# Performance work log

Hardware: AMD Instinct MI355X
Metric: run time of the kernel (lower is better)

The kernel has to match this reference:

```python
import jax, jax.numpy as jnp
from jax import lax
import numpy as np

IN, HID, OUT = 28, 64, 10


def _lstm_layer(x_seq, W_ih, W_hh, b_ih, b_hh):
    # x_seq: [B, T, in]; PyTorch gate order: i, f, g, o (stacked along 4H)
    B = x_seq.shape[0]
    H = W_hh.shape[1]
    # Precompute input projection for all timesteps: [B, T, 4H]
    x_proj = jnp.einsum('bti,gi->btg', x_seq, W_ih) + b_ih + b_hh

    def step(carry, xt):
        h, c = carry
        gates = xt + h @ W_hh.T  # [B, 4H]
        i, f, g, o = jnp.split(gates, 4, axis=-1)
        i = jax.nn.sigmoid(i)
        f = jax.nn.sigmoid(f)
        g = jnp.tanh(g)
        o = jax.nn.sigmoid(o)
        c = f * c + i * g
        h = o * jnp.tanh(c)
        return (h, c), h

    h0 = jnp.zeros((B, H), x_seq.dtype)
    (_, _), hs = lax.scan(step, (h0, h0), jnp.swapaxes(x_proj, 0, 1))
    return jnp.swapaxes(hs, 0, 1)  # [B, T, H]


def setup_inputs() -> dict:
    key = jax.random.key(0)
    ks = jax.random.split(key, 12)
    s_in = 1.0 / np.sqrt(HID)
    u = lambda k, shape: jax.random.uniform(k, shape, jnp.float32, -s_in, s_in)
    return {
        'x': jax.random.normal(ks[0], (16384, 1, 28, 28), jnp.float32),
        'W_ih0': u(ks[1], (4 * HID, IN)),
        'W_hh0': u(ks[2], (4 * HID, HID)),
        'b_ih0': u(ks[3], (4 * HID,)),
        'b_hh0': u(ks[4], (4 * HID,)),
        'W_ih1': u(ks[5], (4 * HID, HID)),
        'W_hh1': u(ks[6], (4 * HID, HID)),
        'b_ih1': u(ks[7], (4 * HID,)),
        'b_hh1': u(ks[8], (4 * HID,)),
        'W_lin': u(ks[9], (OUT, HID)),
        'b_lin': u(ks[10], (OUT,)),
    }


def reference(x, W_ih0, W_hh0, b_ih0, b_hh0, W_ih1, W_hh1, b_ih1, b_hh1, W_lin, b_lin):
    # (N, C, H, W) -> (N, C*H, W): sequence of rows, feature = W = 28
    x = x.reshape(x.shape[0], -1, x.shape[-1])
    h1 = _lstm_layer(x, W_ih0, W_hh0, b_ih0, b_hh0)   # [B, T, 64]
    h2 = _lstm_layer(h1, W_ih1, W_hh1, b_ih1, b_hh1)  # [B, T, 64]
    last = h2[:, -1, :]
    return last @ W_lin.T + b_lin  # [B, 10]
```

## Files before the change

### kernel.cpp

```cpp
#include <hip/hip_runtime.h>


typedef _Float16 half8 __attribute__((ext_vector_type(8)));
typedef float floatx4 __attribute__((ext_vector_type(4)));

#define NFRAG 112
#define WS_BIAS_OFF (NFRAG * 1024)
#define K2 2.8853900817779268f

#if __has_builtin(__builtin_amdgcn_exp2f)
#define EXP2(v) __builtin_amdgcn_exp2f(v)
#else
#define EXP2(v) __expf(0.6931471805599453f * (v))
#endif
#define RCP(v) __builtin_amdgcn_rcpf(v)

__global__ void prep_kernel(const float* __restrict__ Wih0, const float* __restrict__ Whh0,
                            const float* __restrict__ bih0, const float* __restrict__ bhh0,
                            const float* __restrict__ Wih1, const float* __restrict__ Whh1,
                            const float* __restrict__ bih1, const float* __restrict__ bhh1,
                            _Float16* __restrict__ wA, float* __restrict__ wBias) {
    int idx = blockIdx.x * blockDim.x + threadIdx.x;
    if (idx < NFRAG * 512) {
        int f = idx >> 9, slot = idx & 511;
        int lane = slot >> 3, j = slot & 7;
        int mt, kt, layer;
        if (f < 48) { layer = 0; mt = f / 3; kt = f % 3; }
        else        { layer = 1; int f2 = f - 48; mt = f2 >> 2; kt = f2 & 3; }
        int m = mt * 16 + (lane & 15);
        int k = kt * 32 + (lane >> 4) * 8 + j;
        int u = m >> 2, g = m & 3;
        int row = g * 64 + u;
        float v;
        if (layer == 0) {
            if (k < 28)       v = Wih0[row * 28 + k];
            else if (k == 28) v = bih0[row] + bhh0[row];
            else if (k < 32)  v = 0.f;
            else              v = Whh0[row * 64 + (k - 32)];
        } else {
            if (k < 64)       v = Wih1[row * 64 + k];
            else              v = Whh1[row * 64 + (k - 64)];
        }
        float s = (g == 2) ? K2 : -1.4426950408889634f;
        wA[idx] = (_Float16)(v * s);
    } else if (idx < NFRAG * 512 + 256) {
        int m = idx - NFRAG * 512;
        int g = m & 3;
        int row = g * 64 + (m >> 2);
        float s = (g == 2) ? K2 : -1.4426950408889634f;
        wBias[m] = (bih1[row] + bhh1[row]) * s;
    }
}

__device__ __forceinline__ void gate4(const floatx4* acc, float* c,
                                      _Float16* plane, const int* offs) {
    float ei[4], ef[4], eg[4], eo[4];
    #pragma unroll
    for (int i = 0; i < 4; ++i) {
        floatx4 a = acc[i];
        ei[i] = EXP2(a[0]);
        ef[i] = EXP2(a[1]);
        eg[i] = EXP2(a[2]);
        eo[i] = EXP2(a[3]);
    }
    float num[4], rd[4], po[4];
    #pragma unroll
    for (int i = 0; i < 4; ++i) {
        float pi = 1.0f + ei[i];
        float pf = 1.0f + ef[i];
        float pg = 1.0f + eg[i];
        po[i] = 1.0f + eo[i];
        float m = pg * pi;
        num[i] = c[i] * m + (eg[i] - 1.0f) * pf;
        rd[i]  = RCP(pf * m);
    }
    float ec[4];
    #pragma unroll
    for (int i = 0; i < 4; ++i) {
        float cn = num[i] * rd[i];
        c[i] = cn;
        ec[i] = EXP2(K2 * cn);
    }
    #pragma unroll
    for (int i = 0; i < 4; ++i) {
        float r2 = RCP(ec[i] * po[i] + po[i]);
        plane[offs[i]] = (_Float16)((ec[i] - 1.0f) * r2);
    }
}

__launch_bounds__(256, 2)
__global__ void lstm_mfma(const float* __restrict__ x,
                          const _Float16* __restrict__ wA,
                          const float* __restrict__ wBias,
                          const float* __restrict__ Wlin, const float* __restrict__ blin,
                          float* __restrict__ out) {
    __shared__ __align__(16) _Float16 h0p[2][2048];
    __shared__ __align__(16) _Float16 h1p[2][2048];
    __shared__ __align__(16) _Float16 xb[2][1024];
    __shared__ float wlin_s[640];
    __shared__ float blin_s[10];

    const int lane = threadIdx.x;
    const int w    = threadIdx.y;
    const int tid  = w * 64 + lane;
    const int quad = lane >> 4;
    const int col  = lane & 15;
    const int l8   = lane * 8;

    half8 A0[4][3], A1[4][4];
    floatx4 bias1[4];
    int hwr0[4];
    #pragma unroll
    for (int j = 0; j < 4; ++j) {
        const int MT = 4 * w + j;
        #pragma unroll
        for (int kt = 0; kt < 3; ++kt)
            A0[j][kt] = *(const half8*)(wA + (MT * 3 + kt) * 512 + l8);
        #pragma unroll
        for (int kt = 0; kt < 4; ++kt)
            A1[j][kt] = *(const half8*)(wA + (48 + MT * 4 + kt) * 512 + l8);
        const int u = MT * 4 + quad;
        bias1[j] = *(const floatx4*)(wBias + u * 4);
        hwr0[j] = (u >> 5) * 512 + (((u >> 3) & 3) * 16 + col) * 8 + (u & 7);
    }

    const int ks = tid & 31;
    const int cs = tid >> 5;
    const bool xvalid = ks < 28;
    const bool xone   = (ks == 28);
    const float* xg = x + (blockIdx.x * 32 + cs) * 784 + ks;
    const int xstg0 = ((ks >> 3) * 16 + cs) * 8 + (ks & 7);

    {
        #pragma unroll
        for (int k = 0; k < 4; ++k) {
            ((int*)&h0p[1][0])[tid * 4 + k] = 0;
            ((int*)&h1p[1][0])[tid * 4 + k] = 0;
        }
        #pragma unroll
        for (int s = 0; s < 4; ++s) {
            float xv = xvalid ? xg[s * 8 * 784] : 0.f;
            xb[0][xstg0 + (s & 1) * 64 + (s >> 1) * 512] =
                xone ? (_Float16)1.0f : (_Float16)xv;
        }
    }
    __syncthreads();

    float c0[2][4] = {{0.f, 0.f, 0.f, 0.f}, {0.f, 0.f, 0.f, 0.f}};
    float c1[2][4] = {{0.f, 0.f, 0.f, 0.f}, {0.f, 0.f, 0.f, 0.f}};

    for (int p = -1; p <= 27; ++p) {
        const int pr  = p & 1;
        const int pr1 = pr ^ 1;
        const bool doL0 = (p < 27);
        const bool doL1 = (p >= 0);

        float xn[4] = {0.f, 0.f, 0.f, 0.f};
        if (p <= 25 && xvalid) {
            const float* xgp = xg + (p + 2) * 28;
            #pragma unroll
            for (int s = 0; s < 4; ++s) xn[s] = xgp[s * 8 * 784];
        }

        #pragma unroll
        for (int in = 0; in < 2; ++in) {
            const int hb = in * 1024;

            half8 bh0[2];
            #pragma unroll
            for (int kt = 0; kt < 2; ++kt)
                bh0[kt] = *(const half8*)&h0p[pr][hb + kt * 512 + l8];

            int offs[4];
            #pragma unroll
            for (int j = 0; j < 4; ++j) offs[j] = hwr0[j] + hb;

            if (doL0) {
                half8 bx = *(const half8*)&xb[pr1][in * 512 + l8];
                floatx4 acc0[4];
                #pragma unroll
                for (int j = 0; j < 4; ++j) {
                    acc0[j] = __builtin_amdgcn_mfma_f32_16x16x32_f16(
                                  A0[j][0], bx, (floatx4){0.f, 0.f, 0.f, 0.f}, 0, 0, 0);
                    #pragma unroll
                    for (int kt = 0; kt < 2; ++kt)
                        acc0[j] = __builtin_amdgcn_mfma_f32_16x16x32_f16(
                                      A0[j][kt + 1], bh0[kt], acc0[j], 0, 0, 0);
                }
                if (doL1) {
                    floatx4 acc1[4];
                    half8 bh1[2];
                    #pragma unroll
                    for (int kt = 0; kt < 2; ++kt)
                        bh1[kt] = *(const half8*)&h1p[pr1][hb + kt * 512 + l8];
                    #pragma unroll
                    for (int j = 0; j < 4; ++j) {
                        acc1[j] = bias1[j];
                        #pragma unroll
                        for (int kt = 0; kt < 2; ++kt)
                            acc1[j] = __builtin_amdgcn_mfma_f32_16x16x32_f16(
                                          A1[j][kt], bh0[kt], acc1[j], 0, 0, 0);
                        #pragma unroll
                        for (int kt = 0; kt < 2; ++kt)
                            acc1[j] = __builtin_amdgcn_mfma_f32_16x16x32_f16(
                                          A1[j][kt + 2], bh1[kt], acc1[j], 0, 0, 0);
                    }
                    gate4(acc0, c0[in], &h0p[pr1][0], offs);
                    gate4(acc1, c1[in], &h1p[pr][0], offs);
                } else {
                    gate4(acc0, c0[in], &h0p[pr1][0], offs);
                }
            } else {
                floatx4 acc1[4];
                half8 bh1[2];
                #pragma unroll
                for (int kt = 0; kt < 2; ++kt)
                    bh1[kt] = *(const half8*)&h1p[pr1][hb + kt * 512 + l8];
                #pragma unroll
                for (int j = 0; j < 4; ++j) {
                    acc1[j] = bias1[j];
                    #pragma unroll
                    for (int kt = 0; kt < 2; ++kt)
                        acc1[j] = __builtin_amdgcn_mfma_f32_16x16x32_f16(
                                      A1[j][kt], bh0[kt], acc1[j], 0, 0, 0);
                    #pragma unroll
                    for (int kt = 0; kt < 2; ++kt)
                        acc1[j] = __builtin_amdgcn_mfma_f32_16x16x32_f16(
                                      A1[j][kt + 2], bh1[kt], acc1[j], 0, 0, 0);
                }
                gate4(acc1, c1[in], &h1p[pr][0], offs);
            }
        }

        if (p <= 25) {
            #pragma unroll
            for (int s = 0; s < 4; ++s)
                xb[pr][xstg0 + (s & 1) * 64 + (s >> 1) * 512] =
                    xone ? (_Float16)1.0f : (_Float16)xn[s];
        }
        __syncthreads();
    }

    wlin_s[tid]       = Wlin[tid];
    wlin_s[tid + 256] = Wlin[tid + 256];
    if (tid < 128) wlin_s[tid + 512] = Wlin[tid + 512];
    if (tid < 10)  blin_s[tid] = blin[tid];
    __syncthreads();
    for (int e = tid; e < 320; e += 256) {
        int b = e / 10, o = e - b * 10;
        float a = blin_s[o];
        #pragma unroll 8
        for (int uu = 0; uu < 64; ++uu) {
            float hv = (float)h1p[1][((b >> 4) * 2 + (uu >> 5)) * 512 + (((uu >> 3) & 3) * 16 + (b & 15)) * 8 + (uu & 7)];
            a += wlin_s[o * 64 + uu] * hv;
        }
        out[(blockIdx.x * 32 + b) * 10 + o] = a;
    }
}

extern "C" void kernel_launch(void* const* d_in, const int* in_sizes, int n_in,
                              void* d_out, int out_size, void* d_ws, size_t ws_size,
                              hipStream_t stream) {
    const float* x    = (const float*)d_in[0];
    const float* Wih0 = (const float*)d_in[1];
    const float* Whh0 = (const float*)d_in[2];
    const float* bih0 = (const float*)d_in[3];
    const float* bhh0 = (const float*)d_in[4];
    const float* Wih1 = (const float*)d_in[5];
    const float* Whh1 = (const float*)d_in[6];
    const float* bih1 = (const float*)d_in[7];
    const float* bhh1 = (const float*)d_in[8];
    const float* Wlin = (const float*)d_in[9];
    const float* blin = (const float*)d_in[10];
    float* out = (float*)d_out;

    _Float16* wA    = (_Float16*)d_ws;
    float*    wBias = (float*)((char*)d_ws + WS_BIAS_OFF);

    prep_kernel<<<225, 256, 0, stream>>>(Wih0, Whh0, bih0, bhh0,
                                         Wih1, Whh1, bih1, bhh1, wA, wBias);
    lstm_mfma<<<512, dim3(64, 4), 0, stream>>>(x, wA, wBias, Wlin, blin, out);
}
```

Baseline: 177.2 us.

## Split gate rows over 8 waves per block with 16 sequences each

Each block now handles 16 sequences with 8 waves instead of 32 sequences with 4 waves, so each wave owns 2 gate tiles rather than 4. Per-wave weight registers and the serial per-step work shrink, which lets more blocks sit on a CU (launch bounds 512,8) and shortens the recurrent critical path. Layer-0 and layer-1 gate activations are batched into one gate call to interleave the transcendental work. In exchange, each block does fewer MFMAs per barrier, barriers now span twice as many waves, and the register cap from 8 blocks per CU may force spills.

```diff
diff --git a/kernel.cpp b/kernel.cpp
--- a/kernel.cpp
+++ b/kernel.cpp
@@ -52,20 +52,21 @@
     }
 }
 
-__device__ __forceinline__ void gate4(const floatx4* acc, float* c,
-                                      _Float16* plane, const int* offs) {
-    float ei[4], ef[4], eg[4], eo[4];
-    #pragma unroll
-    for (int i = 0; i < 4; ++i) {
+template <int N>
+__device__ __forceinline__ void gate_batch(const floatx4* acc, float* c,
+                                           _Float16* const* planes, const int* offs) {
+    float ei[N], ef[N], eg[N], eo[N];
+    #pragma unroll
+    for (int i = 0; i < N; ++i) {
         floatx4 a = acc[i];
         ei[i] = EXP2(a[0]);
         ef[i] = EXP2(a[1]);
         eg[i] = EXP2(a[2]);
         eo[i] = EXP2(a[3]);
     }
-    float num[4], rd[4], po[4];
-    #pragma unroll
-    for (int i = 0; i < 4; ++i) {
+    float num[N], rd[N], po[N];
+    #pragma unroll
+    for (int i = 0; i < N; ++i) {
         float pi = 1.0f + ei[i];
         float pf = 1.0f + ef[i];
         float pg = 1.0f + eg[i];
@@ -74,29 +75,29 @@
         num[i] = c[i] * m + (eg[i] - 1.0f) * pf;
         rd[i]  = RCP(pf * m);
     }
-    float ec[4];
-    #pragma unroll
-    for (int i = 0; i < 4; ++i) {
+    float ec[N];
+    #pragma unroll
+    for (int i = 0; i < N; ++i) {
         float cn = num[i] * rd[i];
         c[i] = cn;
         ec[i] = EXP2(K2 * cn);
     }
     #pragma unroll
-    for (int i = 0; i < 4; ++i) {
+    for (int i = 0; i < N; ++i) {
         float r2 = RCP(ec[i] * po[i] + po[i]);
-        plane[offs[i]] = (_Float16)((ec[i] - 1.0f) * r2);
-    }
-}
-
-__launch_bounds__(256, 2)
+        planes[i][offs[i]] = (_Float16)((ec[i] - 1.0f) * r2);
+    }
+}
+
+__launch_bounds__(512, 8)
 __global__ void lstm_mfma(const float* __restrict__ x,
                           const _Float16* __restrict__ wA,
                           const float* __restrict__ wBias,
                           const float* __restrict__ Wlin, const float* __restrict__ blin,
                           float* __restrict__ out) {
-    __shared__ __align__(16) _Float16 h0p[2][2048];
-    __shared__ __align__(16) _Float16 h1p[2][2048];
-    __shared__ __align__(16) _Float16 xb[2][1024];
+    __shared__ __align__(16) _Float16 h0p[2][1024];
+    __shared__ __align__(16) _Float16 h1p[2][1024];
+    __shared__ __align__(16) _Float16 xb[2][512];
     __shared__ float wlin_s[640];
     __shared__ float blin_s[10];
 
@@ -107,12 +108,12 @@
     const int col  = lane & 15;
     const int l8   = lane * 8;
 
-    half8 A0[4][3], A1[4][4];
-    floatx4 bias1[4];
-    int hwr0[4];
-    #pragma unroll
-    for (int j = 0; j < 4; ++j) {
-        const int MT = 4 * w + j;
+    half8 A0[2][3], A1[2][4];
+    floatx4 bias1[2];
+    int hwr[2];
+    #pragma unroll
+    for (int j = 0; j < 2; ++j) {
+        const int MT = 2 * w + j;
         #pragma unroll
         for (int kt = 0; kt < 3; ++kt)
             A0[j][kt] = *(const half8*)(wA + (MT * 3 + kt) * 512 + l8);
@@ -121,33 +122,26 @@
             A1[j][kt] = *(const half8*)(wA + (48 + MT * 4 + kt) * 512 + l8);
         const int u = MT * 4 + quad;
         bias1[j] = *(const floatx4*)(wBias + u * 4);
-        hwr0[j] = (u >> 5) * 512 + (((u >> 3) & 3) * 16 + col) * 8 + (u & 7);
+        hwr[j] = (u >> 5) * 512 + (((u >> 3) & 3) * 16 + col) * 8 + (u & 7);
     }
 
     const int ks = tid & 31;
     const int cs = tid >> 5;
     const bool xvalid = ks < 28;
     const bool xone   = (ks == 28);
-    const float* xg = x + (blockIdx.x * 32 + cs) * 784 + ks;
-    const int xstg0 = ((ks >> 3) * 16 + cs) * 8 + (ks & 7);
+    const float* xg = x + (blockIdx.x * 16 + cs) * 784 + ks;
+    const int xstg = ((ks >> 3) * 16 + cs) * 8 + (ks & 7);
 
     {
-        #pragma unroll
-        for (int k = 0; k < 4; ++k) {
-            ((int*)&h0p[1][0])[tid * 4 + k] = 0;
-            ((int*)&h1p[1][0])[tid * 4 + k] = 0;
-        }
-        #pragma unroll
-        for (int s = 0; s < 4; ++s) {
-            float xv = xvalid ? xg[s * 8 * 784] : 0.f;
-            xb[0][xstg0 + (s & 1) * 64 + (s >> 1) * 512] =
-                xone ? (_Float16)1.0f : (_Float16)xv;
-        }
+        ((int*)&h0p[1][0])[tid] = 0;
+        ((int*)&h1p[1][0])[tid] = 0;
+        float xv = xvalid ? xg[0] : 0.f;
+        xb[0][xstg] = xone ? (_Float16)1.0f : (_Float16)xv;
     }
     __syncthreads();
 
-    float c0[2][4] = {{0.f, 0.f, 0.f, 0.f}, {0.f, 0.f, 0.f, 0.f}};
-    float c1[2][4] = {{0.f, 0.f, 0.f, 0.f}, {0.f, 0.f, 0.f, 0.f}};
+    float c0[2] = {0.f, 0.f};
+    float c1[2] = {0.f, 0.f};
 
     for (int p = -1; p <= 27; ++p) {
         const int pr  = p & 1;
@@ -155,106 +149,85 @@
         const bool doL0 = (p < 27);
         const bool doL1 = (p >= 0);
 
-        float xn[4] = {0.f, 0.f, 0.f, 0.f};
-        if (p <= 25 && xvalid) {
-            const float* xgp = xg + (p + 2) * 28;
-            #pragma unroll
-            for (int s = 0; s < 4; ++s) xn[s] = xgp[s * 8 * 784];
-        }
-
+        float xn = 0.f;
+        if (p <= 25 && xvalid) xn = xg[(p + 2) * 28];
+
+        half8 bx, bh0[2];
+        if (doL0) bx = *(const half8*)&xb[pr1][l8];
         #pragma unroll
-        for (int in = 0; in < 2; ++in) {
-            const int hb = in * 1024;
-
-            half8 bh0[2];
-            #pragma unroll
-            for (int kt = 0; kt < 2; ++kt)
-                bh0[kt] = *(const half8*)&h0p[pr][hb + kt * 512 + l8];
-
-            int offs[4];
-            #pragma unroll
-            for (int j = 0; j < 4; ++j) offs[j] = hwr0[j] + hb;
-
-            if (doL0) {
-                half8 bx = *(const half8*)&xb[pr1][in * 512 + l8];
-                floatx4 acc0[4];
-                #pragma unroll
-                for (int j = 0; j < 4; ++j) {
-                    acc0[j] = __builtin_amdgcn_mfma_f32_16x16x32_f16(
-                                  A0[j][0], bx, (floatx4){0.f, 0.f, 0.f, 0.f}, 0, 0, 0);
-                    #pragma unroll
-                    for (int kt = 0; kt < 2; ++kt)
-                        acc0[j] = __builtin_amdgcn_mfma_f32_16x16x32_f16(
-                                      A0[j][kt + 1], bh0[kt], acc0[j], 0, 0, 0);
-                }
-                if (doL1) {
-                    floatx4 acc1[4];
-                    half8 bh1[2];
-                    #pragma unroll
-                    for (int kt = 0; kt < 2; ++kt)
-                        bh1[kt] = *(const half8*)&h1p[pr1][hb + kt * 512 + l8];
-                    #pragma unroll
-                    for (int j = 0; j < 4; ++j) {
-                        acc1[j] = bias1[j];
-                        #pragma unroll
-                        for (int kt = 0; kt < 2; ++kt)
-                            acc1[j] = __builtin_amdgcn_mfma_f32_16x16x32_f16(
-                                          A1[j][kt], bh0[kt], acc1[j], 0, 0, 0);
-                        #pragma unroll
-                        for (int kt = 0; kt < 2; ++kt)
-                            acc1[j] = __builtin_amdgcn_mfma_f32_16x16x32_f16(
-                                          A1[j][kt + 2], bh1[kt], acc1[j], 0, 0, 0);
-                    }
-                    gate4(acc0, c0[in], &h0p[pr1][0], offs);
-                    gate4(acc1, c1[in], &h1p[pr][0], offs);
-                } else {
-                    gate4(acc0, c0[in], &h0p[pr1][0], offs);
-                }
-            } else {
-                floatx4 acc1[4];
-                half8 bh1[2];
+        for (int kt = 0; kt < 2; ++kt)
+            bh0[kt] = *(const half8*)&h0p[pr][kt * 512 + l8];
+
+        floatx4 acc0[2], acc1[2];
+        if (doL0) {
+            #pragma unroll
+            for (int j = 0; j < 2; ++j) {
+                acc0[j] = __builtin_amdgcn_mfma_f32_16x16x32_f16(
+                              A0[j][0], bx, (floatx4){0.f, 0.f, 0.f, 0.f}, 0, 0, 0);
                 #pragma unroll
                 for (int kt = 0; kt < 2; ++kt)
-                    bh1[kt] = *(const half8*)&h1p[pr1][hb + kt * 512 + l8];
+                    acc0[j] = __builtin_amdgcn_mfma_f32_16x16x32_f16(
+                                  A0[j][kt + 1], bh0[kt], acc0[j], 0, 0, 0);
+            }
+        }
+        if (doL1) {
+            #pragma unroll
+            for (int j = 0; j < 2; ++j) {
+                acc1[j] = bias1[j];
                 #pragma unroll
-                for (int j = 0; j < 4; ++j) {
-                    acc1[j] = bias1[j];
-                    #pragma unroll
-                    for (int kt = 0; kt < 2; ++kt)
-                        acc1[j] = __builtin_amdgcn_mfma_f32_16x16x32_f16(
-                                      A1[j][kt], bh0[kt], acc1[j], 0, 0, 0);
-                    #pragma unroll
-                    for (int kt = 0; kt < 2; ++kt)
-                        acc1[j] = __builtin_amdgcn_mfma_f32_16x16x32_f16(
-                                      A1[j][kt + 2], bh1[kt], acc1[j], 0, 0, 0);
-                }
-                gate4(acc1, c1[in], &h1p[pr][0], offs);
+                for (int kt = 0; kt < 2; ++kt)
+                    acc1[j] = __builtin_amdgcn_mfma_f32_16x16x32_f16(
+                                  A1[j][kt], bh0[kt], acc1[j], 0, 0, 0);
             }
-        }
-
-        if (p <= 25) {
-            #pragma unroll
-            for (int s = 0; s < 4; ++s)
-                xb[pr][xstg0 + (s & 1) * 64 + (s >> 1) * 512] =
-                    xone ? (_Float16)1.0f : (_Float16)xn[s];
-        }
+            half8 bh1[2];
+            #pragma unroll
+            for (int kt = 0; kt < 2; ++kt)
+                bh1[kt] = *(const half8*)&h1p[pr1][kt * 512 + l8];
+            #pragma unroll
+            for (int j = 0; j < 2; ++j)
+                #pragma unroll
+                for (int kt = 0; kt < 2; ++kt)
+                    acc1[j] = __builtin_amdgcn_mfma_f32_16x16x32_f16(
+                                  A1[j][kt + 2], bh1[kt], acc1[j], 0, 0, 0);
+        }
+
+        if (doL0 && doL1) {
+            floatx4 a4[4] = {acc0[0], acc0[1], acc1[0], acc1[1]};
+            float   cc[4] = {c0[0], c0[1], c1[0], c1[1]};
+            _Float16* pl[4] = {h0p[pr1], h0p[pr1], h1p[pr], h1p[pr]};
+            int offs[4] = {hwr[0], hwr[1], hwr[0], hwr[1]};
+            gate_batch<4>(a4, cc, pl, offs);
+            c0[0] = cc[0]; c0[1] = cc[1]; c1[0] = cc[2]; c1[1] = cc[3];
+        } else if (doL0) {
+            floatx4 a2[2] = {acc0[0], acc0[1]};
+            _Float16* pl[2] = {h0p[pr1], h0p[pr1]};
+            int offs[2] = {hwr[0], hwr[1]};
+            gate_batch<2>(a2, c0, pl, offs);
+        } else {
+            floatx4 a2[2] = {acc1[0], acc1[1]};
+            _Float16* pl[2] = {h1p[pr], h1p[pr]};
+            int offs[2] = {hwr[0], hwr[1]};
+            gate_batch<2>(a2, c1, pl, offs);
+        }
+
+        if (p <= 25)
+            xb[pr][xstg] = xone ? (_Float16)1.0f : (_Float16)xn;
         __syncthreads();
     }
 
-    wlin_s[tid]       = Wlin[tid];
-    wlin_s[tid + 256] = Wlin[tid + 256];
-    if (tid < 128) wlin_s[tid + 512] = Wlin[tid + 512];
+    wlin_s[tid] = Wlin[tid];
+    if (tid < 128) wlin_s[512 + tid] = Wlin[512 + tid];
     if (tid < 10)  blin_s[tid] = blin[tid];
     __syncthreads();
-    for (int e = tid; e < 320; e += 256) {
-        int b = e / 10, o = e - b * 10;
+    if (tid < 160) {
+        int b = tid / 10, o = tid - b * 10;
         float a = blin_s[o];
         #pragma unroll 8
         for (int uu = 0; uu < 64; ++uu) {
-            float hv = (float)h1p[1][((b >> 4) * 2 + (uu >> 5)) * 512 + (((uu >> 3) & 3) * 16 + (b & 15)) * 8 + (uu & 7)];
+            float hv = (float)h1p[1][(uu >> 5) * 512 + (((uu >> 3) & 3) * 16 + b) * 8 + (uu & 7)];
             a += wlin_s[o * 64 + uu] * hv;
         }
-        out[(blockIdx.x * 32 + b) * 10 + o] = a;
+        out[(blockIdx.x * 16 + b) * 10 + o] = a;
     }
 }
 
@@ -279,5 +252,5 @@
 
     prep_kernel<<<225, 256, 0, stream>>>(Wih0, Whh0, bih0, bhh0,
                                          Wih1, Whh1, bih1, bhh1, wA, wBias);
-    lstm_mfma<<<512, dim3(64, 4), 0, stream>>>(x, wA, wBias, Wlin, blin, out);
-}
+    lstm_mfma<<<1024, dim3(64, 8), 0, stream>>>(x, wA, wBias, Wlin, blin, out);
+}
```

After: 444.7 us. 151% more time.
